# Performance work log

Hardware: AMD Instinct MI355X
Metric: run time of the kernel (lower is better)

Reference implementation:

```python
import jax, jax.numpy as jnp
import numpy as np

IN_DIM = 14400
K = 25
DIMS = [7200, 3600, 1800]  # floor(in_dim / 2**(i+1))
OUT_DIM = 2
BATCH = 256


def setup_inputs() -> dict:
    key = jax.random.key(0)
    ks = jax.random.split(key, 32)
    inp = {}
    inp["x"] = jax.random.normal(ks[0], (BATCH, 2 * IN_DIM), dtype=jnp.float32)
    # shared KNN tables (both channels load the same h5 files)
    prev = [IN_DIM] + DIMS[:-1]
    for i, (d, p) in enumerate(zip(DIMS, prev)):
        inp[f"knn{i}"] = jax.random.randint(ks[1 + i], (d, K), 0, p, dtype=jnp.int64)
    std = (2.0 / K) ** 0.5
    kidx = 4
    for ch in ("p", "n"):
        for i, d in enumerate(DIMS):
            inp[f"w{ch}{i}"] = jax.random.normal(ks[kidx], (d, K), dtype=jnp.float32) * std; kidx += 1
            inp[f"b{ch}{i}"] = jnp.zeros((1, d), dtype=jnp.float32)
        inp[f"fc{ch}_w"] = jax.random.normal(ks[kidx], (OUT_DIM, DIMS[-1]), dtype=jnp.float32) * (1.0 / DIMS[-1] ** 0.5); kidx += 1
        inp[f"fc{ch}_b"] = jnp.zeros((OUT_DIM,), dtype=jnp.float32)
    inp["fc3_w"] = jax.random.normal(ks[kidx], (OUT_DIM, 4), dtype=jnp.float32) * 0.5
    inp["fc3_b"] = jnp.zeros((OUT_DIM,), dtype=jnp.float32)
    return inp


def _lcn(x, knns, ws, bs, fw, fb):
    # x: (B, in_dim). Each layer: gather KNN neighbors, weighted sum, bias, relu.
    for knn, w, b in zip(knns, ws, bs):
        g = x[:, knn]                                  # (B, dim, K) gather
        x = jax.nn.relu(jnp.einsum('bdk,dk->bd', g, w) + b)
    return x @ fw.T + fb                               # fc_angle


def reference(x, knn0, knn1, knn2,
              wp0, bp0, wp1, bp1, wp2, bp2, fcp_w, fcp_b,
              wn0, bn0, wn1, bn1, wn2, bn2, fcn_w, fcn_b,
              fc3_w, fc3_b):
    knns = (knn0, knn1, knn2)
    xpos = _lcn(x[:, :IN_DIM], knns, (wp0, wp1, wp2), (bp0, bp1, bp2), fcp_w, fcp_b)
    xneg = _lcn(x[:, IN_DIM:], knns, (wn0, wn1, wn2), (bn0, bn1, bn2), fcn_w, fcn_b)
    h = jax.nn.relu(jnp.concatenate([xpos, xneg], axis=1))  # (B, 4)
    return h @ fc3_w.T + fc3_b
```

## Files before the change

kernel.cpp:

```cpp
#include <hip/hip_runtime.h>
#include <hip/hip_bf16.h>

using bf16 = __hip_bfloat16;

#define K 25
#define D0 7200
#define D1 3600
#define D2 1800

#define PKB_L1 360000
#define PKB_L2 540000
#define NPK    630000
#define PBB_L1 14400
#define PBB_L2 21600
#define NPB    25200

#define NT 512

__device__ __forceinline__ float b2f(ushort u) {
  unsigned int w = ((unsigned int)u) << 16;
  float f; __builtin_memcpy(&f, &w, 4); return f;
}
__device__ __forceinline__ ushort f2b(float f) {
  bf16 h = __float2bfloat16(f);
  ushort u; __builtin_memcpy(&u, &h, 2); return u;
}

__global__ __launch_bounds__(256) void prepack_kernel(
    const void* __restrict__ x,
    const void* __restrict__ knn0, const void* __restrict__ knn1,
    const void* __restrict__ knn2,
    const void* __restrict__ wp0, const void* __restrict__ bp0,
    const void* __restrict__ wp1, const void* __restrict__ bp1,
    const void* __restrict__ wp2, const void* __restrict__ bp2,
    const void* __restrict__ wn0, const void* __restrict__ bn0,
    const void* __restrict__ wn1, const void* __restrict__ bn1,
    const void* __restrict__ wn2, const void* __restrict__ bn2,
    unsigned int* __restrict__ pk, float* __restrict__ pbias,
    float* __restrict__ y, int* __restrict__ flags) {
  __shared__ int s_flags[2];
  const int t = threadIdx.x;
  if (t < 64) {
    const unsigned int u = ((const unsigned int*)x)[t * 997];
    const unsigned int e = (u >> 23) & 0xFF;
    const unsigned long long m = __ballot((e >= 192) || (e <= 30));
    if (t == 0) s_flags[0] = (__popcll(m) >= 32) ? 1 : 0;
  } else if (t < 128) {
    const int l = t - 64;
    const unsigned int hi = ((const unsigned int*)knn0)[2 * l + 1];
    const unsigned long long m = __ballot(hi != 0);
    if (l == 0) s_flags[1] = (m == 0ULL) ? 1 : 0;
  }
  __syncthreads();
  const int fdt = s_flags[0], idt = s_flags[1];

  if (blockIdx.x == 0 && t == 0) {
    flags[0] = fdt; flags[1] = idt; flags[16] = 0;
  }

  const int gid = blockIdx.x * 256 + t;
  if (gid < NPK) {
    int i = gid, ch, k, d, dout;
    const void *kn, *wsel;
    if (i < PKB_L1) {
      ch = i / 180000; i -= ch * 180000; dout = D0; kn = knn0;
      wsel = ch ? wn0 : wp0;
    } else if (i < PKB_L2) {
      i -= PKB_L1; ch = i / 90000; i -= ch * 90000; dout = D1; kn = knn1;
      wsel = ch ? wn1 : wp1;
    } else {
      i -= PKB_L2; ch = i / 45000; i -= ch * 45000; dout = D2; kn = knn2;
      wsel = ch ? wn2 : wp2;
    }
    k = i / dout; d = i - k * dout;
    const int pos = d * K + k;
    const unsigned int idx = idt ? ((const unsigned int*)kn)[2 * pos]
                                 : ((const unsigned int*)kn)[pos];
    const ushort wb = fdt ? ((const ushort*)wsel)[pos]
                          : f2b(((const float*)wsel)[pos]);
    pk[gid] = (idx << 16) | (unsigned int)wb;
  } else if (gid < NPK + NPB) {
    int i = gid - NPK, ch, d;
    const void* src;
    if (i < PBB_L1) {
      ch = i / D0; d = i - ch * D0; src = ch ? bn0 : bp0;
    } else if (i < PBB_L2) {
      const int i2 = i - PBB_L1; ch = i2 / D1; d = i2 - ch * D1; src = ch ? bn1 : bp1;
    } else {
      const int i2 = i - PBB_L2; ch = i2 / D2; d = i2 - ch * D2; src = ch ? bn2 : bp2;
    }
    pbias[i] = fdt ? b2f(((const ushort*)src)[d]) : ((const float*)src)[d];
  } else if (gid < NPK + NPB + 1024) {
    y[gid - (NPK + NPB)] = 0.0f;
  }
}

__device__ __forceinline__ void layer_run(ushort* lds, const unsigned int* __restrict__ pk,
                                          const float* __restrict__ pbias,
                                          int offIn, int offOut, int pkb, int pbb,
                                          int dout) {
  for (int d = threadIdx.x; d < dout; d += NT) {
    const unsigned int* s = pk + pkb + d;
    float a0 = 0.f, a1 = 0.f;
#pragma unroll
    for (int k = 0; k < K; ++k) {
      const unsigned int pw = s[k * dout];
      const unsigned int vv = *(const unsigned int*)&lds[offIn + ((pw >> 16) << 1)];
      const float w = b2f((ushort)(pw & 0xFFFFu));
      a0 = fmaf(w, b2f((ushort)(vv & 0xFFFFu)), a0);
      a1 = fmaf(w, b2f((ushort)(vv >> 16)), a1);
    }
    const float bias = pbias[pbb + d];
    a0 = fmaxf(a0 + bias, 0.f);
    a1 = fmaxf(a1 + bias, 0.f);
    *(unsigned int*)&lds[offOut + (d << 1)] =
        (unsigned int)f2b(a0) | ((unsigned int)f2b(a1) << 16);
  }
}

__global__ __launch_bounds__(NT) void lcn_fused(
    const void* __restrict__ x, const unsigned int* __restrict__ pk,
    const float* __restrict__ pbias,
    const void* __restrict__ fcpw, const void* __restrict__ fcnw,
    const void* __restrict__ fcpb, const void* __restrict__ fcnb,
    const void* __restrict__ f3w, const void* __restrict__ f3b,
    float* __restrict__ y, int* __restrict__ flags, void* __restrict__ out) {
  __shared__ ushort lds[43200];
  __shared__ float red[NT / 64][4];
  __shared__ int sflag;
  const int t = threadIdx.x;
  const int ch = blockIdx.x & 1;
  const int b0 = (blockIdx.x >> 1) * 2;

  if (t == 0) sflag = flags[0];
  __syncthreads();
  const int fdt = sflag;

  if (fdt) {
    const ushort* r0 = (const ushort*)x + (size_t)b0 * 28800 + ch * 14400;
    const ushort* r1 = r0 + 28800;
    for (int c = t; c < 3600; c += NT) {
      const ushort4 a = ((const ushort4*)r0)[c];
      const ushort4 b = ((const ushort4*)r1)[c];
      unsigned int* dst = (unsigned int*)&lds[c * 8];
      dst[0] = (unsigned int)a.x | ((unsigned int)b.x << 16);
      dst[1] = (unsigned int)a.y | ((unsigned int)b.y << 16);
      dst[2] = (unsigned int)a.z | ((unsigned int)b.z << 16);
      dst[3] = (unsigned int)a.w | ((unsigned int)b.w << 16);
    }
  } else {
    const float* r0 = (const float*)x + (size_t)b0 * 28800 + ch * 14400;
    const float* r1 = r0 + 28800;
    for (int c = t; c < 3600; c += NT) {
      const float4 a = ((const float4*)r0)[c];
      const float4 b = ((const float4*)r1)[c];
      unsigned int* dst = (unsigned int*)&lds[c * 8];
      dst[0] = (unsigned int)f2b(a.x) | ((unsigned int)f2b(b.x) << 16);
      dst[1] = (unsigned int)f2b(a.y) | ((unsigned int)f2b(b.y) << 16);
      dst[2] = (unsigned int)f2b(a.z) | ((unsigned int)f2b(b.z) << 16);
      dst[3] = (unsigned int)f2b(a.w) | ((unsigned int)f2b(b.w) << 16);
    }
  }
  __syncthreads();

  layer_run(lds, pk, pbias, 0, 28800, 0 + ch * 180000, 0 + ch * D0, D0);
  __syncthreads();
  layer_run(lds, pk, pbias, 28800, 0, PKB_L1 + ch * 90000, PBB_L1 + ch * D1, D1);
  __syncthreads();
  layer_run(lds, pk, pbias, 0, 7200, PKB_L2 + ch * 45000, PBB_L2 + ch * D2, D2);
  __syncthreads();

  {
    const void* fw = ch ? fcnw : fcpw;
    float a00 = 0.f, a01 = 0.f, a10 = 0.f, a11 = 0.f;
    for (int d = t; d < D2; d += NT) {
      const unsigned int vv = *(const unsigned int*)&lds[7200 + (d << 1)];
      const float v0 = b2f((ushort)(vv & 0xFFFFu));
      const float v1 = b2f((ushort)(vv >> 16));
      const float w0 = fdt ? b2f(((const ushort*)fw)[d]) : ((const float*)fw)[d];
      const float w1 = fdt ? b2f(((const ushort*)fw)[D2 + d]) : ((const float*)fw)[D2 + d];
      a00 = fmaf(w0, v0, a00); a01 = fmaf(w0, v1, a01);
      a10 = fmaf(w1, v0, a10); a11 = fmaf(w1, v1, a11);
    }
#pragma unroll
    for (int off = 32; off > 0; off >>= 1) {
      a00 += __shfl_down(a00, off);
      a01 += __shfl_down(a01, off);
      a10 += __shfl_down(a10, off);
      a11 += __shfl_down(a11, off);
    }
    const int wave = t >> 6, lane = t & 63;
    if (lane == 0) {
      red[wave][0] = a00; red[wave][1] = a01; red[wave][2] = a10; red[wave][3] = a11;
    }
    __syncthreads();
    if (t == 0) {
      float s00 = 0.f, s01 = 0.f, s10 = 0.f, s11 = 0.f;
#pragma unroll
      for (int wv = 0; wv < NT / 64; ++wv) {
        s00 += red[wv][0]; s01 += red[wv][1]; s10 += red[wv][2]; s11 += red[wv][3];
      }
      atomicAdd(&y[(ch * 2 + 0) * 256 + b0], s00);
      atomicAdd(&y[(ch * 2 + 0) * 256 + b0 + 1], s01);
      atomicAdd(&y[(ch * 2 + 1) * 256 + b0], s10);
      atomicAdd(&y[(ch * 2 + 1) * 256 + b0 + 1], s11);
    }
  }

  __syncthreads();
  if (t == 0) {
    __threadfence();
    sflag = (atomicAdd(&flags[16], 1) == (int)gridDim.x - 1) ? 1 : 0;
  }
  __syncthreads();
  if (sflag && t < 256) {
    const int b = t;
    const float y0 = atomicAdd(&y[0 * 256 + b], 0.0f);
    const float y1 = atomicAdd(&y[1 * 256 + b], 0.0f);
    const float y2 = atomicAdd(&y[2 * 256 + b], 0.0f);
    const float y3 = atomicAdd(&y[3 * 256 + b], 0.0f);
    const float bp0v = fdt ? b2f(((const ushort*)fcpb)[0]) : ((const float*)fcpb)[0];
    const float bp1v = fdt ? b2f(((const ushort*)fcpb)[1]) : ((const float*)fcpb)[1];
    const float bn0v = fdt ? b2f(((const ushort*)fcnb)[0]) : ((const float*)fcnb)[0];
    const float bn1v = fdt ? b2f(((const ushort*)fcnb)[1]) : ((const float*)fcnb)[1];
    const float h0v = fmaxf(y0 + bp0v, 0.f);
    const float h1v = fmaxf(y1 + bp1v, 0.f);
    const float h2v = fmaxf(y2 + bn0v, 0.f);
    const float h3v = fmaxf(y3 + bn1v, 0.f);
#pragma unroll
    for (int o = 0; o < 2; ++o) {
      float w0, w1, w2, w3, bb;
      if (fdt) {
        const ushort* fp = (const ushort*)f3w;
        w0 = b2f(fp[o * 4 + 0]); w1 = b2f(fp[o * 4 + 1]);
        w2 = b2f(fp[o * 4 + 2]); w3 = b2f(fp[o * 4 + 3]);
        bb = b2f(((const ushort*)f3b)[o]);
      } else {
        const float* fp = (const float*)f3w;
        w0 = fp[o * 4 + 0]; w1 = fp[o * 4 + 1];
        w2 = fp[o * 4 + 2]; w3 = fp[o * 4 + 3];
        bb = ((const float*)f3b)[o];
      }
      float r = bb;
      r = fmaf(w0, h0v, r); r = fmaf(w1, h1v, r);
      r = fmaf(w2, h2v, r); r = fmaf(w3, h3v, r);
      if (fdt) ((ushort*)out)[b * 2 + o] = f2b(r);
      else     ((float*)out)[b * 2 + o] = r;
    }
  }
}

extern "C" void kernel_launch(void* const* d_in, const int* in_sizes, int n_in,
                              void* d_out, int out_size, void* d_ws, size_t ws_size,
                              hipStream_t stream) {
  const void* x    = d_in[0];
  const void* knn0 = d_in[1];
  const void* knn1 = d_in[2];
  const void* knn2 = d_in[3];
  const void* wp0  = d_in[4];  const void* bp0 = d_in[5];
  const void* wp1  = d_in[6];  const void* bp1 = d_in[7];
  const void* wp2  = d_in[8];  const void* bp2 = d_in[9];
  const void* fcpw = d_in[10]; const void* fcpb = d_in[11];
  const void* wn0  = d_in[12]; const void* bn0 = d_in[13];
  const void* wn1  = d_in[14]; const void* bn1 = d_in[15];
  const void* wn2  = d_in[16]; const void* bn2 = d_in[17];
  const void* fcnw = d_in[18]; const void* fcnb = d_in[19];
  const void* f3w  = d_in[20]; const void* f3b  = d_in[21];

  char* ws = (char*)d_ws;
  unsigned int* pk = (unsigned int*)(ws);
  float* pbias = (float*)(ws + 2520000);
  float* y     = (float*)(ws + 2620800);
  int* flags   = (int*)(ws + 2624896);

  prepack_kernel<<<2564, 256, 0, stream>>>(x, knn0, knn1, knn2,
                                           wp0, bp0, wp1, bp1, wp2, bp2,
                                           wn0, bn0, wn1, bn1, wn2, bn2,
                                           pk, pbias, y, flags);

  lcn_fused<<<256, NT, 0, stream>>>(x, pk, pbias, fcpw, fcnw, fcpb, fcnb,
                                    f3w, f3b, y, flags, d_out);
}
```

Baseline: 152.0 us.

## Restructure prepack to one thread per output row and double fused block size

The prepack kernel now assigns one thread per output neuron, which loops over its 25 neighbors and also writes that neuron's bias. The launch drops from 2564 blocks to 103, cutting launch and index-math overhead. Separately, the fused LCN kernel's thread count per block goes from 512 to 1024 to raise parallelism in the gather-sum loops. The prepack now reads the KNN and weight tables with strided, uncoalesced loads across only about 26K threads, which may hurt memory efficiency. The larger block may also raise register pressure.

```diff
diff --git a/kernel.cpp b/kernel.cpp
--- a/kernel.cpp
+++ b/kernel.cpp
@@ -11,11 +11,9 @@
 #define PKB_L1 360000
 #define PKB_L2 540000
 #define NPK    630000
-#define PBB_L1 14400
-#define PBB_L2 21600
 #define NPB    25200
 
-#define NT 512
+#define NT 1024
 
 __device__ __forceinline__ float b2f(ushort u) {
   unsigned int w = ((unsigned int)u) << 16;
@@ -59,39 +57,34 @@
   }
 
   const int gid = blockIdx.x * 256 + t;
-  if (gid < NPK) {
-    int i = gid, ch, k, d, dout;
-    const void *kn, *wsel;
-    if (i < PKB_L1) {
-      ch = i / 180000; i -= ch * 180000; dout = D0; kn = knn0;
-      wsel = ch ? wn0 : wp0;
-    } else if (i < PKB_L2) {
-      i -= PKB_L1; ch = i / 90000; i -= ch * 90000; dout = D1; kn = knn1;
-      wsel = ch ? wn1 : wp1;
+  if (gid < NPB) {
+    int i = gid, d, dout, pkb;
+    const void *kn, *wsel, *bsel;
+    if (i < 14400) {
+      const int ch = i / D0; d = i - ch * D0; dout = D0;
+      pkb = ch * 180000; kn = knn0;
+      wsel = ch ? wn0 : wp0; bsel = ch ? bn0 : bp0;
+    } else if (i < 21600) {
+      i -= 14400; const int ch = i / D1; d = i - ch * D1; dout = D1;
+      pkb = PKB_L1 + ch * 90000; kn = knn1;
+      wsel = ch ? wn1 : wp1; bsel = ch ? bn1 : bp1;
     } else {
-      i -= PKB_L2; ch = i / 45000; i -= ch * 45000; dout = D2; kn = knn2;
-      wsel = ch ? wn2 : wp2;
-    }
-    k = i / dout; d = i - k * dout;
-    const int pos = d * K + k;
-    const unsigned int idx = idt ? ((const unsigned int*)kn)[2 * pos]
-                                 : ((const unsigned int*)kn)[pos];
-    const ushort wb = fdt ? ((const ushort*)wsel)[pos]
-                          : f2b(((const float*)wsel)[pos]);
-    pk[gid] = (idx << 16) | (unsigned int)wb;
-  } else if (gid < NPK + NPB) {
-    int i = gid - NPK, ch, d;
-    const void* src;
-    if (i < PBB_L1) {
-      ch = i / D0; d = i - ch * D0; src = ch ? bn0 : bp0;
-    } else if (i < PBB_L2) {
-      const int i2 = i - PBB_L1; ch = i2 / D1; d = i2 - ch * D1; src = ch ? bn1 : bp1;
-    } else {
-      const int i2 = i - PBB_L2; ch = i2 / D2; d = i2 - ch * D2; src = ch ? bn2 : bp2;
-    }
-    pbias[i] = fdt ? b2f(((const ushort*)src)[d]) : ((const float*)src)[d];
-  } else if (gid < NPK + NPB + 1024) {
-    y[gid - (NPK + NPB)] = 0.0f;
+      i -= 21600; const int ch = i / D2; d = i - ch * D2; dout = D2;
+      pkb = PKB_L2 + ch * 45000; kn = knn2;
+      wsel = ch ? wn2 : wp2; bsel = ch ? bn2 : bp2;
+    }
+    const int pos0 = d * K;
+#pragma unroll
+    for (int k = 0; k < K; ++k) {
+      const unsigned int idx = idt ? ((const unsigned int*)kn)[2 * (pos0 + k)]
+                                   : ((const unsigned int*)kn)[pos0 + k];
+      const ushort wb = fdt ? ((const ushort*)wsel)[pos0 + k]
+                            : f2b(((const float*)wsel)[pos0 + k]);
+      pk[pkb + k * dout + d] = (idx << 16) | (unsigned int)wb;
+    }
+    pbias[gid] = fdt ? b2f(((const ushort*)bsel)[d]) : ((const float*)bsel)[d];
+  } else if (gid < NPB + 1024) {
+    y[gid - NPB] = 0.0f;
   }
 }
 
@@ -165,9 +158,9 @@
 
   layer_run(lds, pk, pbias, 0, 28800, 0 + ch * 180000, 0 + ch * D0, D0);
   __syncthreads();
-  layer_run(lds, pk, pbias, 28800, 0, PKB_L1 + ch * 90000, PBB_L1 + ch * D1, D1);
-  __syncthreads();
-  layer_run(lds, pk, pbias, 0, 7200, PKB_L2 + ch * 45000, PBB_L2 + ch * D2, D2);
+  layer_run(lds, pk, pbias, 28800, 0, PKB_L1 + ch * 90000, 14400 + ch * D1, D1);
+  __syncthreads();
+  layer_run(lds, pk, pbias, 0, 7200, PKB_L2 + ch * 45000, 21600 + ch * D2, D2);
   __syncthreads();
 
   {
@@ -273,10 +266,10 @@
   float* y     = (float*)(ws + 2620800);
   int* flags   = (int*)(ws + 2624896);
 
-  prepack_kernel<<<2564, 256, 0, stream>>>(x, knn0, knn1, knn2,
-                                           wp0, bp0, wp1, bp1, wp2, bp2,
-                                           wn0, bn0, wn1, bn1, wn2, bn2,
-                                           pk, pbias, y, flags);
+  prepack_kernel<<<103, 256, 0, stream>>>(x, knn0, knn1, knn2,
+                                          wp0, bp0, wp1, bp1, wp2, bp2,
+                                          wn0, bn0, wn1, bn1, wn2, bn2,
+                                          pk, pbias, y, flags);
 
   lcn_fused<<<256, NT, 0, stream>>>(x, pk, pbias, fcpw, fcnw, fcpb, fcnb,
                                     f3w, f3b, y, flags, d_out);
```

New measurement: 147.8 us. 2.8% less time.
